# Performance work log

Measured on AMD Instinct MI355X. Metric: run time of the kernel, lower is better.

The kernel has to match this reference:

```python
import jax, jax.numpy as jnp
import numpy as np

NUM_HEADS = 12
EPS = 1e-6


def _rms_norm(x, w):
    # RMSNorm over the full channel dim (applied before head split), fp32 math
    return x * jax.lax.rsqrt(jnp.mean(x * x, axis=-1, keepdims=True) + EPS) * w


def _rope_apply(t, F, H, W, freqs):
    # t: [B, S, n, d] with S == F*H*W; freqs: [1024, d//2] angles
    B, S, n, d = t.shape
    c = d // 2
    s0 = c - 2 * (c // 3)  # temporal split (22 when d=128)
    s1 = c // 3            # spatial splits (21, 21)
    f0, f1, f2 = freqs[:, :s0], freqs[:, s0:s0 + s1], freqs[:, s0 + s1:]
    ang = jnp.concatenate([
        jnp.broadcast_to(f0[:F, None, None, :], (F, H, W, s0)),
        jnp.broadcast_to(f1[None, :H, None, :], (F, H, W, s1)),
        jnp.broadcast_to(f2[None, None, :W, :], (F, H, W, s1)),
    ], axis=-1).reshape(S, c)                      # [S, c]
    cos = jnp.cos(ang)[None, :, None, :]           # [1, S, 1, c]
    sin = jnp.sin(ang)[None, :, None, :]
    tp = t.reshape(B, S, n, c, 2)
    te, to = tp[..., 0], tp[..., 1]                # complex (real, imag) pairs
    rot = jnp.stack([te * cos - to * sin, te * sin + to * cos], axis=-1)
    return rot.reshape(B, S, n, d)


def reference(x, seq_lens, grid_sizes, freqs, Wq, bq, Wk, bk, Wv, bv, Wo, bo, norm_q_w, norm_k_w):
    B, S, C = x.shape
    n = NUM_HEADS
    d = C // n
    gs = np.asarray(grid_sizes)[0]
    F, H, W = int(gs[0]), int(gs[1]), int(gs[2])  # static: L == F*H*W, same per sample

    q = _rms_norm(x @ Wq.T + bq, norm_q_w).reshape(B, S, n, d)
    k = _rms_norm(x @ Wk.T + bk, norm_k_w).reshape(B, S, n, d)
    v = (x @ Wv.T + bv).reshape(B, S, n, d)

    q = _rope_apply(q, F, H, W, freqs)
    k = _rope_apply(k, F, H, W, freqs)

    scale = 1.0 / jnp.sqrt(jnp.float32(d))
    scores = jnp.einsum('bqnd,bknd->bnqk', q, k) * scale   # [B, n, S, S]
    kmask = jnp.arange(S)[None, :] < seq_lens[:, None]      # [B, S] valid keys
    scores = jnp.where(kmask[:, None, None, :], scores, -jnp.inf)
    attn = jax.nn.softmax(scores, axis=-1)
    out = jnp.einsum('bnqk,bknd->bqnd', attn, v).reshape(B, S, C)
    return out @ Wo.T + bo


def setup_inputs() -> dict:
    key = jax.random.key(0)
    ks = jax.random.split(key, 10)
    B, F, H, W = 2, 4, 24, 32
    S = F * H * W  # 3072
    C = 1536
    d = C // NUM_HEADS  # 128
    c = d // 2          # 64

    x = jax.random.normal(ks[0], (B, S, C), dtype=jnp.float32)
    seq_lens = jnp.array([S, 2500], dtype=jnp.int32)
    grid_sizes = jnp.array([[F, H, W]] * B, dtype=jnp.int32)

    # rope angles: outer(pos, 1/theta^(2i/dim)) per split [22, 21, 21]
    def rope_params(max_len, dim_k, theta=10000.0):
        inv = 1.0 / (theta ** (np.arange(0, dim_k, 2, dtype=np.float64) / dim_k))
        return np.outer(np.arange(max_len), inv)
    s0 = c - 2 * (c // 3)
    s1 = c // 3
    freqs = jnp.asarray(np.concatenate([
        rope_params(1024, 2 * s0), rope_params(1024, 2 * s1), rope_params(1024, 2 * s1)
    ], axis=1), dtype=jnp.float32)  # [1024, 64]

    std = 0.02
    def lin(k):
        return jax.random.normal(k, (C, C), dtype=jnp.float32) * std
    return {
        'x': x, 'seq_lens': seq_lens, 'grid_sizes': grid_sizes, 'freqs': freqs,
        'Wq': lin(ks[1]), 'bq': jnp.zeros((C,), jnp.float32),
        'Wk': lin(ks[2]), 'bk': jnp.zeros((C,), jnp.float32),
        'Wv': lin(ks[3]), 'bv': jnp.zeros((C,), jnp.float32),
        'Wo': lin(ks[4]), 'bo': jnp.zeros((C,), jnp.float32),
        'norm_q_w': jnp.ones((C,), jnp.float32),
        'norm_k_w': jnp.ones((C,), jnp.float32),
    }
```

## Files before the change

kernel.cpp:

```cpp
#include <hip/hip_runtime.h>
#include <math.h>

#define NB 2
#define SS 3072
#define CC 1536
#define NH 12
#define DH 128
#define NTOK (NB * SS)
#define WE (CC * CC)
#define LOG2E 1.4426950408889634f

typedef __attribute__((ext_vector_type(8))) short short8;
typedef __attribute__((ext_vector_type(4))) float floatx4;

#define GLOAD(g, l) __builtin_amdgcn_global_load_lds( \
    (const __attribute__((address_space(1))) void*)(g), \
    (__attribute__((address_space(3))) void*)(l), 16, 0, 0)

__device__ __forceinline__ unsigned short f2bf(float f) {
    unsigned u = __float_as_uint(f);
    u += 0x7fffu + ((u >> 16) & 1u);
    return (unsigned short)(u >> 16);
}
__device__ __forceinline__ int swz(int row, int q) {
    return row * 4 + (q ^ ((row >> 1) & 3));
}

__global__ __launch_bounds__(256) void cast_all(
    const float* __restrict__ x,
    const float* __restrict__ w0, const float* __restrict__ w1,
    const float* __restrict__ w2, const float* __restrict__ w3,
    unsigned short* __restrict__ o)
{
    const int y = blockIdx.y;
    const float* src = (y < 4) ? x + (size_t)y * WE
                     : (y == 4) ? w0 : (y == 5) ? w1 : (y == 6) ? w2 : w3;
    size_t i = ((size_t)blockIdx.x * 256 + threadIdx.x) * 4;
    float4 v = *(const float4*)&src[i];
    uint2 u;
    u.x = (unsigned)f2bf(v.x) | ((unsigned)f2bf(v.y) << 16);
    u.y = (unsigned)f2bf(v.z) | ((unsigned)f2bf(v.w) << 16);
    *(uint2*)&o[(size_t)y * WE + i] = u;
}

__global__ __launch_bounds__(256) void rope_table(
    const float* __restrict__ freqs, const int* __restrict__ gsz,
    float2* __restrict__ tab)
{
    const int id = blockIdx.x * 256 + threadIdx.x;
    const int s = id >> 6, pj = id & 63;
    const int Hg = gsz[1], Wg = gsz[2];
    const int f = s / (Hg * Wg);
    const int rem = s - f * Hg * Wg;
    const int hh = rem / Wg;
    const int ww = rem - hh * Wg;
    const int row = (pj < 22) ? f : ((pj < 43) ? hh : ww);
    float sn, cs;
    sincosf(freqs[row * 64 + pj], &sn, &cs);
    tab[id] = make_float2(cs, sn);
}

__global__ __launch_bounds__(256) void qkv_gemm(
    const unsigned short* __restrict__ X,
    const unsigned short* __restrict__ Wqb, const unsigned short* __restrict__ Wkb,
    const unsigned short* __restrict__ Wvb,
    const float* __restrict__ bq, const float* __restrict__ bk,
    const float* __restrict__ bv,
    unsigned short* __restrict__ qo, unsigned short* __restrict__ ko,
    unsigned short* __restrict__ vto)
{
    __shared__ unsigned short As[128 * 32];
    __shared__ unsigned short Bs[128 * 32];
    const int tid = threadIdx.x;
    const int w = tid >> 6, l = tid & 63;
    const int jseg = blockIdx.y / 12;
    const unsigned short* Wt = (jseg == 0) ? Wqb : (jseg == 1) ? Wkb : Wvb;
    const float* bias        = (jseg == 0) ? bq  : (jseg == 1) ? bk  : bv;
    unsigned short* Y        = (jseg == 0) ? qo  : (jseg == 1) ? ko  : vto;
    const int i0 = blockIdx.x * 128, j0 = (blockIdx.y % 12) * 128;
    const int srow = tid >> 2;
    const int gk8 = (((tid & 3) ^ ((srow >> 1) & 3))) * 8;

    floatx4 acc[4][4] = {};
    for (int k0 = 0; k0 < CC; k0 += 32) {
        __syncthreads();
        GLOAD(X + (size_t)(i0 + srow) * CC + k0 + gk8,        As + (size_t)tid * 8);
        GLOAD(X + (size_t)(i0 + 64 + srow) * CC + k0 + gk8,   As + (size_t)(256 + tid) * 8);
        GLOAD(Wt + (size_t)(j0 + srow) * CC + k0 + gk8,       Bs + (size_t)tid * 8);
        GLOAD(Wt + (size_t)(j0 + 64 + srow) * CC + k0 + gk8,  Bs + (size_t)(256 + tid) * 8);
        __syncthreads();
        const int wr = (w >> 1) * 64, wc = (w & 1) * 64;
        short8 af[4], bf[4];
        #pragma unroll
        for (int mb = 0; mb < 4; ++mb)
            af[mb] = *(const short8*)&As[swz(wr + mb * 16 + (l & 15), l >> 4) * 8];
        #pragma unroll
        for (int nb = 0; nb < 4; ++nb)
            bf[nb] = *(const short8*)&Bs[swz(wc + nb * 16 + (l & 15), l >> 4) * 8];
        #pragma unroll
        for (int mb = 0; mb < 4; ++mb)
            #pragma unroll
            for (int nb = 0; nb < 4; ++nb)
                acc[mb][nb] = __builtin_amdgcn_mfma_f32_16x16x32_bf16(
                    af[mb], bf[nb], acc[mb][nb], 0, 0, 0);
    }

    const int wr = (w >> 1) * 64, wc = (w & 1) * 64;
    #pragma unroll
    for (int mb = 0; mb < 4; ++mb)
        #pragma unroll
        for (int nb = 0; nb < 4; ++nb) {
            const int n = j0 + wc + nb * 16 + (l & 15);
            const float bv2 = bias[n];
            const int h = n >> 7, td = n & 127;
            #pragma unroll
            for (int r = 0; r < 4; ++r) {
                const int m = i0 + wr + mb * 16 + (l >> 4) * 4 + r;
                const float val = acc[mb][nb][r] + bv2;
                const int b = (m >= SS) ? 1 : 0;
                const int s = m - b * SS;
                if (jseg < 2)
                    Y[((size_t)(b * NH + h) * SS + s) * DH + td] = f2bf(val);
                else
                    Y[((size_t)(b * NH + h) * DH + td) * SS + s] = f2bf(val);
            }
        }
}

__global__ __launch_bounds__(256) void gemm_o(
    const unsigned short* __restrict__ X, const unsigned short* __restrict__ Wt,
    const float* __restrict__ bias, float* __restrict__ Y)
{
    __shared__ unsigned short As[128 * 32];
    __shared__ unsigned short Bs[128 * 32];
    const int tid = threadIdx.x;
    const int w = tid >> 6, l = tid & 63;
    const int i0 = blockIdx.x * 128, j0 = blockIdx.y * 128;
    const int srow = tid >> 2;
    const int gk8 = (((tid & 3) ^ ((srow >> 1) & 3))) * 8;

    floatx4 acc[4][4] = {};
    for (int k0 = 0; k0 < CC; k0 += 32) {
        __syncthreads();
        GLOAD(X + (size_t)(i0 + srow) * CC + k0 + gk8,        As + (size_t)tid * 8);
        GLOAD(X + (size_t)(i0 + 64 + srow) * CC + k0 + gk8,   As + (size_t)(256 + tid) * 8);
        GLOAD(Wt + (size_t)(j0 + srow) * CC + k0 + gk8,       Bs + (size_t)tid * 8);
        GLOAD(Wt + (size_t)(j0 + 64 + srow) * CC + k0 + gk8,  Bs + (size_t)(256 + tid) * 8);
        __syncthreads();
        const int wr = (w >> 1) * 64, wc = (w & 1) * 64;
        short8 af[4], bf[4];
        #pragma unroll
        for (int mb = 0; mb < 4; ++mb)
            af[mb] = *(const short8*)&As[swz(wr + mb * 16 + (l & 15), l >> 4) * 8];
        #pragma unroll
        for (int nb = 0; nb < 4; ++nb)
            bf[nb] = *(const short8*)&Bs[swz(wc + nb * 16 + (l & 15), l >> 4) * 8];
        #pragma unroll
        for (int mb = 0; mb < 4; ++mb)
            #pragma unroll
            for (int nb = 0; nb < 4; ++nb)
                acc[mb][nb] = __builtin_amdgcn_mfma_f32_16x16x32_bf16(
                    af[mb], bf[nb], acc[mb][nb], 0, 0, 0);
    }

    const int wr = (w >> 1) * 64, wc = (w & 1) * 64;
    #pragma unroll
    for (int mb = 0; mb < 4; ++mb)
        #pragma unroll
        for (int nb = 0; nb < 4; ++nb) {
            const int n = j0 + wc + nb * 16 + (l & 15);
            const float bv = bias[n];
            #pragma unroll
            for (int r = 0; r < 4; ++r) {
                const int m = i0 + wr + mb * 16 + (l >> 4) * 4 + r;
                Y[(size_t)m * CC + n] = acc[mb][nb][r] + bv;
            }
        }
}

__global__ __launch_bounds__(256) void norm_rope(
    unsigned short* __restrict__ qb, unsigned short* __restrict__ kb,
    const float* __restrict__ nqw, const float* __restrict__ nkw,
    const float2* __restrict__ tab)
{
    const int bid = blockIdx.x;
    const int which = (bid >= NTOK) ? 1 : 0;
    const int tok = bid - which * NTOK;
    unsigned short* t    = which ? kb : qb;
    const float* wgt     = which ? nkw : nqw;
    const float outscale = which ? 1.0f : 0.08838834764831845f * LOG2E;
    const int b = tok / SS, s = tok - b * SS;
    const int tid = threadIdx.x;

    float2 vals[3];
    size_t addrs[3];
    float ss = 0.f;
    #pragma unroll
    for (int kt = 0; kt < 3; ++kt) {
        int p = tid + kt * 256;
        int h = p >> 6, pj = p & 63;
        size_t addr = ((size_t)(b * NH + h) * SS + s) * DH + 2 * pj;
        addrs[kt] = addr;
        unsigned u = *(const unsigned*)&t[addr];
        float2 v;
        v.x = __uint_as_float(u << 16);
        v.y = __uint_as_float(u & 0xffff0000u);
        vals[kt] = v;
        ss += v.x * v.x + v.y * v.y;
    }
    #pragma unroll
    for (int off = 32; off > 0; off >>= 1) ss += __shfl_down(ss, off, 64);
    __shared__ float red[4];
    if ((tid & 63) == 0) red[tid >> 6] = ss;
    __syncthreads();
    const float total = red[0] + red[1] + red[2] + red[3];
    const float rstd = rsqrtf(total * (1.0f / CC) + 1e-6f) * outscale;

    #pragma unroll
    for (int kt = 0; kt < 3; ++kt) {
        int p = tid + kt * 256;
        int h = p >> 6, pj = p & 63;
        float2 cssn = tab[s * 64 + pj];
        int ch = h * DH + 2 * pj;
        float te = vals[kt].x * rstd * wgt[ch];
        float to = vals[kt].y * rstd * wgt[ch + 1];
        unsigned o = (unsigned)f2bf(te * cssn.x - to * cssn.y) |
                     ((unsigned)f2bf(te * cssn.y + to * cssn.x) << 16);
        *(unsigned*)&t[addrs[kt]] = o;
    }
}

__global__ __launch_bounds__(256, 2) void flash_attn_mfma(
    const unsigned short* __restrict__ qg, const unsigned short* __restrict__ kg,
    const unsigned short* __restrict__ vg, const int* __restrict__ seq_lens,
    unsigned short* __restrict__ out)
{
    __shared__ unsigned short Qs[128 * 128];
    __shared__ unsigned short Ks[64 * 128];
    __shared__ unsigned short Vs[128 * 64];

    const int tid = threadIdx.x;
    const int w = tid >> 6, l = tid & 63;
    const int bid = blockIdx.x;
    const int qt = bid / (NB * NH);
    const int rem0 = bid - qt * (NB * NH);
    const int h = rem0 >> 1;
    const int b = rem0 & 1;
    const int slen = seq_lens[b];
    const int s0 = qt * 128;

    const unsigned short* qbase = qg + ((size_t)(b * NH + h) * SS + s0) * DH;
    const unsigned short* kbase = kg + ((size_t)(b * NH + h) * SS) * DH;
    const unsigned short* vbase = vg + ((size_t)(b * NH + h) * DH) * SS;
    unsigned short* Psw = Qs + (size_t)w * (32 * 72);

    #pragma unroll
    for (int i = 0; i < 8; ++i) {
        int cid = i * 256 + tid;
        int kc = cid >> 9, r2 = cid & 511, row = r2 >> 2, sq = r2 & 3;
        GLOAD(qbase + (size_t)row * DH + kc * 32 + (sq ^ ((row >> 1) & 3)) * 8,
              Qs + (size_t)cid * 8);
    }
    __syncthreads();
    short8 qf[2][4];
    #pragma unroll
    for (int rb = 0; rb < 2; ++rb)
        #pragma unroll
        for (int kc = 0; kc < 4; ++kc)
            qf[rb][kc] = *(const short8*)&Qs[(kc * 512 + swz(w * 32 + rb * 16 + (l & 15), l >> 4)) * 8];

    floatx4 acc[2][8] = {};
    float lsum[2][4] = {};
    const int ntiles = (slen + 63) >> 6;

    for (int kt = 0; kt < ntiles; ++kt) {
        __syncthreads();
        #pragma unroll
        for (int i = 0; i < 4; ++i) {
            int cid = i * 256 + tid;
            int kc = cid >> 8, r2 = cid & 255, row = r2 >> 2, sq = r2 & 3;
            GLOAD(kbase + (size_t)(kt * 64 + row) * DH + kc * 32 + (sq ^ ((row >> 1) & 3)) * 8,
                  Ks + (size_t)cid * 8);
        }
        #pragma unroll
        for (int i = 0; i < 4; ++i) {
            int cid = i * 256 + tid;
            int ks = cid >> 9, r2 = cid & 511, dc = r2 >> 2, sq = r2 & 3;
            GLOAD(vbase + (size_t)dc * SS + kt * 64 + ks * 32 + (sq ^ ((dc >> 1) & 3)) * 8,
                  Vs + (size_t)cid * 8);
        }
        __syncthreads();

        floatx4 sv[2][4] = {};
        #pragma unroll
        for (int kc = 0; kc < 4; ++kc) {
            short8 kf[4];
            #pragma unroll
            for (int nb = 0; nb < 4; ++nb)
                kf[nb] = *(const short8*)&Ks[(kc * 256 + swz(nb * 16 + (l & 15), l >> 4)) * 8];
            #pragma unroll
            for (int rb = 0; rb < 2; ++rb)
                #pragma unroll
                for (int nb = 0; nb < 4; ++nb)
                    sv[rb][nb] = __builtin_amdgcn_mfma_f32_16x16x32_bf16(
                        qf[rb][kc], kf[nb], sv[rb][nb], 0, 0, 0);
        }

        const int valid = slen - kt * 64;
        #pragma unroll
        for (int rb = 0; rb < 2; ++rb) {
            if (valid >= 64) {
                #pragma unroll
                for (int nb = 0; nb < 4; ++nb)
                    #pragma unroll
                    for (int r = 0; r < 4; ++r)
                        sv[rb][nb][r] = exp2f(sv[rb][nb][r]);
            } else {
                #pragma unroll
                for (int nb = 0; nb < 4; ++nb) {
                    const int key = nb * 16 + (l & 15);
                    #pragma unroll
                    for (int r = 0; r < 4; ++r)
                        sv[rb][nb][r] = (key < valid) ? exp2f(sv[rb][nb][r]) : 0.0f;
                }
            }
            #pragma unroll
            for (int r = 0; r < 4; ++r)
                lsum[rb][r] += sv[rb][0][r] + sv[rb][1][r] + sv[rb][2][r] + sv[rb][3][r];
            #pragma unroll
            for (int nb = 0; nb < 4; ++nb)
                #pragma unroll
                for (int r = 0; r < 4; ++r)
                    Psw[(rb * 16 + (l >> 4) * 4 + r) * 72 + nb * 16 + (l & 15)] =
                        f2bf(sv[rb][nb][r]);
        }

        #pragma unroll
        for (int ks = 0; ks < 2; ++ks) {
            short8 pa[2];
            #pragma unroll
            for (int rb = 0; rb < 2; ++rb)
                pa[rb] = *(const short8*)&Psw[(rb * 16 + (l & 15)) * 72 + ks * 32 + (l >> 4) * 8];
            #pragma unroll
            for (int nb2 = 0; nb2 < 8; ++nb2) {
                short8 vf = *(const short8*)&Vs[(ks * 512 + swz(nb2 * 16 + (l & 15), l >> 4)) * 8];
                #pragma unroll
                for (int rb = 0; rb < 2; ++rb)
                    acc[rb][nb2] = __builtin_amdgcn_mfma_f32_16x16x32_bf16(
                        pa[rb], vf, acc[rb][nb2], 0, 0, 0);
            }
        }
    }

    #pragma unroll
    for (int rb = 0; rb < 2; ++rb) {
        float rl[4];
        #pragma unroll
        for (int r = 0; r < 4; ++r) {
            float s = lsum[rb][r];
            #pragma unroll
            for (int mm = 1; mm < 16; mm <<= 1) s += __shfl_xor(s, mm, 64);
            rl[r] = 1.0f / s;
        }
        #pragma unroll
        for (int nb2 = 0; nb2 < 8; ++nb2) {
            const int col = h * DH + nb2 * 16 + (l & 15);
            #pragma unroll
            for (int r = 0; r < 4; ++r) {
                const int srow = s0 + w * 32 + rb * 16 + (l >> 4) * 4 + r;
                out[((size_t)b * SS + srow) * CC + col] = f2bf(acc[rb][nb2][r] * rl[r]);
            }
        }
    }
}

extern "C" void kernel_launch(void* const* d_in, const int* in_sizes, int n_in,
                              void* d_out, int out_size, void* d_ws, size_t ws_size,
                              hipStream_t stream) {
    const float* x          = (const float*)d_in[0];
    const int*   seq_lens   = (const int*)d_in[1];
    const int*   grid_sizes = (const int*)d_in[2];
    const float* freqs      = (const float*)d_in[3];
    const float* Wq         = (const float*)d_in[4];
    const float* bq         = (const float*)d_in[5];
    const float* Wk         = (const float*)d_in[6];
    const float* bk         = (const float*)d_in[7];
    const float* Wv         = (const float*)d_in[8];
    const float* bv         = (const float*)d_in[9];
    const float* Wo         = (const float*)d_in[10];
    const float* bo         = (const float*)d_in[11];
    const float* nqw        = (const float*)d_in[12];
    const float* nkw        = (const float*)d_in[13];
    float* out = (float*)d_out;

    const size_t TE = (size_t)NTOK * CC;
    unsigned short* xb  = (unsigned short*)d_ws;
    unsigned short* wqb = xb + TE;
    unsigned short* wkb = wqb + WE;
    unsigned short* wvb = wkb + WE;
    unsigned short* wob = wvb + WE;
    unsigned short* qb  = wob + WE;
    unsigned short* kb  = qb + TE;
    unsigned short* vtb = kb + TE;
    unsigned short* ab  = vtb + TE;
    float2* tab = (float2*)(ab + TE);

    cast_all<<<dim3(WE / 1024, 8), 256, 0, stream>>>(x, Wq, Wk, Wv, Wo, xb);
    rope_table<<<dim3(SS * 64 / 256), 256, 0, stream>>>(freqs, grid_sizes, tab);

    qkv_gemm<<<dim3(NTOK / 128, 36), 256, 0, stream>>>(
        xb, wqb, wkb, wvb, bq, bk, bv, qb, kb, vtb);

    norm_rope<<<dim3(2 * NTOK), 256, 0, stream>>>(qb, kb, nqw, nkw, tab);

    flash_attn_mfma<<<dim3(NB * NH * (SS / 128)), 256, 0, stream>>>(qb, kb, vtb, seq_lens, ab);

    gemm_o<<<dim3(NTOK / 128, CC / 128), 256, 0, stream>>>(ab, wob, bo, out);
}
```

Baseline: 560.0 us.

## Register-prefetch next K/V tile and give P scratch its own LDS region

The direct global-to-LDS loads of K and V are replaced by register staging: the next tile is loaded into registers while the current tile is computed, then written to LDS at the start of the following iteration. LDS is merged into one buffer, with the P scratch area moved out of the Q region into a dedicated slice. The P bf16 conversion now uses a packed two-element intrinsic. The goal is to hide global load latency behind the MFMA work, at the cost of 32 extra VGPRs, which may hurt occupancy under launch_bounds(256,2), plus extra LDS write instructions.

Result: slower. 791.9 us (+41.4%).

```diff
diff --git a/kernel.cpp b/kernel.cpp
--- a/kernel.cpp
+++ b/kernel.cpp
@@ -1,4 +1,5 @@
 #include <hip/hip_runtime.h>
+#include <hip/hip_bf16.h>
 #include <math.h>
 
 #define NB 2
@@ -235,12 +236,13 @@
     const unsigned short* __restrict__ vg, const int* __restrict__ seq_lens,
     unsigned short* __restrict__ out)
 {
-    __shared__ unsigned short Qs[128 * 128];
-    __shared__ unsigned short Ks[64 * 128];
-    __shared__ unsigned short Vs[128 * 64];
-
+    __shared__ unsigned short lds[25600];
+    unsigned short* Ks = lds;
+    unsigned short* Vs = lds + 8192;
     const int tid = threadIdx.x;
     const int w = tid >> 6, l = tid & 63;
+    unsigned short* Psw = lds + 16384 + w * (32 * 72);
+
     const int bid = blockIdx.x;
     const int qt = bid / (NB * NH);
     const int rem0 = bid - qt * (NB * NH);
@@ -252,14 +254,13 @@
     const unsigned short* qbase = qg + ((size_t)(b * NH + h) * SS + s0) * DH;
     const unsigned short* kbase = kg + ((size_t)(b * NH + h) * SS) * DH;
     const unsigned short* vbase = vg + ((size_t)(b * NH + h) * DH) * SS;
-    unsigned short* Psw = Qs + (size_t)w * (32 * 72);
 
     #pragma unroll
     for (int i = 0; i < 8; ++i) {
         int cid = i * 256 + tid;
         int kc = cid >> 9, r2 = cid & 511, row = r2 >> 2, sq = r2 & 3;
         GLOAD(qbase + (size_t)row * DH + kc * 32 + (sq ^ ((row >> 1) & 3)) * 8,
-              Qs + (size_t)cid * 8);
+              lds + (size_t)cid * 8);
     }
     __syncthreads();
     short8 qf[2][4];
@@ -267,7 +268,28 @@
     for (int rb = 0; rb < 2; ++rb)
         #pragma unroll
         for (int kc = 0; kc < 4; ++kc)
-            qf[rb][kc] = *(const short8*)&Qs[(kc * 512 + swz(w * 32 + rb * 16 + (l & 15), l >> 4)) * 8];
+            qf[rb][kc] = *(const short8*)&lds[(kc * 512 + swz(w * 32 + rb * 16 + (l & 15), l >> 4)) * 8];
+
+    int koff[4], voff[4];
+    #pragma unroll
+    for (int i = 0; i < 4; ++i) {
+        int cid = i * 256 + tid;
+        {
+            int kc = cid >> 8, r2 = cid & 255, row = r2 >> 2, sq = r2 & 3;
+            koff[i] = row * DH + kc * 32 + (sq ^ ((row >> 1) & 3)) * 8;
+        }
+        {
+            int ks = cid >> 9, r2 = cid & 511, dc = r2 >> 2, sq = r2 & 3;
+            voff[i] = dc * SS + ks * 32 + (sq ^ ((dc >> 1) & 3)) * 8;
+        }
+    }
+
+    uint4 kreg[4], vreg[4];
+    #pragma unroll
+    for (int i = 0; i < 4; ++i) {
+        kreg[i] = *(const uint4*)(kbase + koff[i]);
+        vreg[i] = *(const uint4*)(vbase + voff[i]);
+    }
 
     floatx4 acc[2][8] = {};
     float lsum[2][4] = {};
@@ -278,16 +300,17 @@
         #pragma unroll
         for (int i = 0; i < 4; ++i) {
             int cid = i * 256 + tid;
-            int kc = cid >> 8, r2 = cid & 255, row = r2 >> 2, sq = r2 & 3;
-            GLOAD(kbase + (size_t)(kt * 64 + row) * DH + kc * 32 + (sq ^ ((row >> 1) & 3)) * 8,
-                  Ks + (size_t)cid * 8);
-        }
-        #pragma unroll
-        for (int i = 0; i < 4; ++i) {
-            int cid = i * 256 + tid;
-            int ks = cid >> 9, r2 = cid & 511, dc = r2 >> 2, sq = r2 & 3;
-            GLOAD(vbase + (size_t)dc * SS + kt * 64 + ks * 32 + (sq ^ ((dc >> 1) & 3)) * 8,
-                  Vs + (size_t)cid * 8);
+            *(uint4*)&Ks[(size_t)cid * 8] = kreg[i];
+            *(uint4*)&Vs[(size_t)cid * 8] = vreg[i];
+        }
+        if (kt + 1 < ntiles) {
+            const unsigned short* kb2 = kbase + (size_t)(kt + 1) * 64 * DH;
+            const unsigned short* vb2 = vbase + (size_t)(kt + 1) * 64;
+            #pragma unroll
+            for (int i = 0; i < 4; ++i) {
+                kreg[i] = *(const uint4*)(kb2 + koff[i]);
+                vreg[i] = *(const uint4*)(vb2 + voff[i]);
+            }
         }
         __syncthreads();
 
@@ -330,9 +353,14 @@
             #pragma unroll
             for (int nb = 0; nb < 4; ++nb)
                 #pragma unroll
-                for (int r = 0; r < 4; ++r)
-                    Psw[(rb * 16 + (l >> 4) * 4 + r) * 72 + nb * 16 + (l & 15)] =
-                        f2bf(sv[rb][nb][r]);
+                for (int r = 0; r < 4; r += 2) {
+                    union { __hip_bfloat162 v; ushort2 u; } cv;
+                    cv.v = __float22bfloat162_rn(
+                        make_float2(sv[rb][nb][r], sv[rb][nb][r + 1]));
+                    const int rowb = rb * 16 + (l >> 4) * 4 + r;
+                    Psw[rowb * 72 + nb * 16 + (l & 15)]       = cv.u.x;
+                    Psw[(rowb + 1) * 72 + nb * 16 + (l & 15)] = cv.u.y;
+                }
         }
 
         #pragma unroll
```
